# Optimization experiments

Hardware: AMD Instinct MI355X
Metric: run time of the kernel (lower is better)

Reference implementation:

```python
import jax, jax.numpy as jnp
import numpy as np

V, E, H, T = 50000, 128, 256, 9
H2 = H // 2
B, S = 128, 512


def setup_inputs() -> dict:
    key = jax.random.key(0)
    ks = jax.random.split(key, 12)
    sc = 0.05
    return {
        "x": jax.random.randint(ks[0], (B, S), 0, V, dtype=jnp.int64) if False else jax.random.randint(ks[0], (B, S), 0, V).astype(jnp.int64),
        "mask": jnp.ones((B, S), dtype=jnp.int32),
        "embed": jax.random.normal(ks[1], (V, E), jnp.float32) * sc,
        "W_ih_f": jax.random.normal(ks[2], (4 * H2, E), jnp.float32) * sc,
        "W_hh_f": jax.random.normal(ks[3], (4 * H2, H2), jnp.float32) * sc,
        "b_f": jax.random.normal(ks[4], (4 * H2,), jnp.float32) * sc,
        "W_ih_b": jax.random.normal(ks[5], (4 * H2, E), jnp.float32) * sc,
        "W_hh_b": jax.random.normal(ks[6], (4 * H2, H2), jnp.float32) * sc,
        "b_b": jax.random.normal(ks[7], (4 * H2,), jnp.float32) * sc,
        "W_out": jax.random.normal(ks[8], (T, H), jnp.float32) * sc,
        "b_out": jax.random.normal(ks[9], (T,), jnp.float32) * sc,
        "start_trans": jax.random.normal(ks[10], (T,), jnp.float32) * sc,
        "trans": jax.random.normal(ks[11], (T, T), jnp.float32) * sc,
        "end_trans": jax.random.normal(jax.random.fold_in(key, 99), (T,), jnp.float32) * sc,
    }


def _lstm_dir(xg, W_hh, reverse):
    # xg: [B,S,4*H2] precomputed input projections (+bias)
    if reverse:
        xg = xg[:, ::-1]
    b = xg.shape[0]
    h0 = jnp.zeros((b, H2), xg.dtype)

    def step(carry, xt):
        h, c = carry
        g = xt + h @ W_hh.T
        i, f, gg, o = jnp.split(g, 4, axis=-1)
        c = jax.nn.sigmoid(f) * c + jax.nn.sigmoid(i) * jnp.tanh(gg)
        h = jax.nn.sigmoid(o) * jnp.tanh(c)
        return (h, c), h

    _, hs = jax.lax.scan(step, (h0, h0), jnp.swapaxes(xg, 0, 1))
    hs = jnp.swapaxes(hs, 0, 1)  # [B,S,H2]
    if reverse:
        hs = hs[:, ::-1]
    return hs


def _emissions(x, embed, W_ih_f, W_hh_f, b_f, W_ih_b, W_hh_b, b_b, W_out, b_out):
    emb = embed[x]  # [B,S,E]
    xg_f = jnp.einsum('bse,ge->bsg', emb, W_ih_f) + b_f
    xg_b = jnp.einsum('bse,ge->bsg', emb, W_ih_b) + b_b
    h_f = _lstm_dir(xg_f, W_hh_f, False)
    h_b = _lstm_dir(xg_b, W_hh_b, True)
    feats = jnp.concatenate([h_f, h_b], axis=-1)  # [B,S,H]
    return jnp.einsum('bsh,th->bst', feats, W_out) + b_out  # [B,S,T]


def _viterbi(emissions, mask, start_trans, trans, end_trans):
    # emissions [B,S,T], mask [B,S] (1 = valid prefix)
    m = mask.astype(bool)
    score0 = start_trans + emissions[:, 0]  # [B,T]

    def fwd_step(score, inp):
        em_t, m_t = inp  # [B,T], [B]
        nxt = score[:, :, None] + trans[None] + em_t[:, None, :]  # [B,prev,next]
        best = nxt.max(axis=1)
        idx = nxt.argmax(axis=1).astype(jnp.int32)  # [B,T] backpointers
        score = jnp.where(m_t[:, None], best, score)
        return score, idx

    em_rest = jnp.swapaxes(emissions[:, 1:], 0, 1)  # [S-1,B,T]
    m_rest = jnp.swapaxes(m[:, 1:], 0, 1)  # [S-1,B]
    score, history = jax.lax.scan(fwd_step, score0, (em_rest, m_rest))
    final = score + end_trans
    best_scores = final.max(axis=-1)  # [B]
    cur = final.argmax(axis=-1).astype(jnp.int32)  # [B] tag at last valid step

    def back_step(cur, inp):
        hist_t, m_t = inp  # [B,T], [B]
        tag = jnp.where(m_t, cur, -1)  # -1 pads positions beyond seq end
        prev = jnp.take_along_axis(hist_t, cur[:, None], axis=1)[:, 0]
        cur = jnp.where(m_t, prev, cur)
        return cur, tag

    cur0, tags_rev = jax.lax.scan(back_step, cur, (history[::-1], m_rest[::-1]))
    paths = jnp.concatenate(
        [cur0[:, None], jnp.swapaxes(tags_rev, 0, 1)[:, ::-1]], axis=1)  # [B,S]
    return paths, best_scores


def reference(x, mask, embed, W_ih_f, W_hh_f, b_f, W_ih_b, W_hh_b, b_b,
              W_out, b_out, start_trans, trans, end_trans):
    emissions = _emissions(x, embed, W_ih_f, W_hh_f, b_f,
                           W_ih_b, W_hh_b, b_b, W_out, b_out)
    paths, best_scores = _viterbi(emissions, mask, start_trans, trans, end_trans)
    return paths, best_scores
```

## Files before the change

kernel.cpp:

```cpp
#include <hip/hip_runtime.h>
#include <stdint.h>

#define S_LEN 512
#define NT 9

typedef __attribute__((ext_vector_type(8)))  short          bf16x8;
typedef __attribute__((ext_vector_type(4)))  float          f32x4;
typedef __attribute__((ext_vector_type(4)))  unsigned short u16x4;

static __device__ __forceinline__ unsigned short f2bf(float f) {
    union { float f; unsigned u; } c; c.f = f;
    return (unsigned short)((c.u + 0x7fffu + ((c.u >> 16) & 1u)) >> 16);
}
static __device__ __forceinline__ float bf2f(unsigned short h) {
    union { unsigned u; float f; } c; c.u = ((unsigned)h) << 16;
    return c.f;
}
static __device__ __forceinline__ bf16x8 cvt8(const float* p) {
    f32x4 a = *(const f32x4*)p, b = *(const f32x4*)(p + 4);
    bf16x8 fr;
    fr[0]=(short)f2bf(a[0]); fr[1]=(short)f2bf(a[1]); fr[2]=(short)f2bf(a[2]); fr[3]=(short)f2bf(a[3]);
    fr[4]=(short)f2bf(b[0]); fr[5]=(short)f2bf(b[1]); fr[6]=(short)f2bf(b[2]); fr[7]=(short)f2bf(b[3]);
    return fr;
}
static __device__ __forceinline__ bf16x8 pack8(f32x4 a, f32x4 b) {
    bf16x8 fr;
    fr[0]=(short)f2bf(a[0]); fr[1]=(short)f2bf(a[1]); fr[2]=(short)f2bf(a[2]); fr[3]=(short)f2bf(a[3]);
    fr[4]=(short)f2bf(b[0]); fr[5]=(short)f2bf(b[1]); fr[6]=(short)f2bf(b[2]); fr[7]=(short)f2bf(b[3]);
    return fr;
}
static __device__ __forceinline__ float sigf(float x) {
    return __builtin_amdgcn_rcpf(1.0f + __expf(-x));
}
static __device__ __forceinline__ float tanhf_(float x) {
    return 1.0f - 2.0f * __builtin_amdgcn_rcpf(1.0f + __expf(2.0f * x));
}

static __device__ __forceinline__ void wg_barrier_lds() {
    asm volatile("s_waitcnt lgkmcnt(0)" ::: "memory");
    __builtin_amdgcn_s_barrier();
    asm volatile("" ::: "memory");
}

__global__ __launch_bounds__(512) void k_eg(
    const float* __restrict__ embed,
    const float* __restrict__ Wf, const float* __restrict__ bF,
    const float* __restrict__ Wb, const float* __restrict__ bB,
    unsigned short* __restrict__ eg)
{
    const int dir = blockIdx.y, wg = blockIdx.x;
    const float* __restrict__ W    = dir ? Wb : Wf;
    const float* __restrict__ bias = dir ? bB : bF;
    const int tid = threadIdx.x;
    const int wv = tid >> 6, L = tid & 63, l15 = L & 15, l4 = L >> 4;

    bf16x8 Bf[4][4];
    float  bq[4];
#pragma unroll
    for (int q = 0; q < 4; ++q) {
        const int gate = q * 128 + wv * 16 + l15;
        bq[q] = bias[gate];
#pragma unroll
        for (int kt = 0; kt < 4; ++kt)
            Bf[q][kt] = cvt8(W + gate * 128 + kt * 32 + l4 * 8);
    }

    const int vt0 = wg * 25;
    const int hc  = wv * 16 + l15;
    const float* ap = embed + (size_t)(vt0 * 16 + l15) * 128 + l4 * 8;

    f32x4 pv[8];
#pragma unroll
    for (int kt = 0; kt < 4; ++kt) {
        pv[2*kt]   = *(const f32x4*)(ap + kt * 32);
        pv[2*kt+1] = *(const f32x4*)(ap + kt * 32 + 4);
    }

    for (int i = 0; i < 25; ++i) {
        bf16x8 A[4];
#pragma unroll
        for (int kt = 0; kt < 4; ++kt)
            A[kt] = pack8(pv[2*kt], pv[2*kt+1]);
        if (i < 24) {
            const float* apn = ap + (size_t)(i + 1) * 2048;
#pragma unroll
            for (int kt = 0; kt < 4; ++kt) {
                pv[2*kt]   = *(const f32x4*)(apn + kt * 32);
                pv[2*kt+1] = *(const f32x4*)(apn + kt * 32 + 4);
            }
        }
        f32x4 acc[4];
#pragma unroll
        for (int q = 0; q < 4; ++q) {
            f32x4 a0 = { bq[q], bq[q], bq[q], bq[q] };
#pragma unroll
            for (int kt = 0; kt < 4; ++kt)
                a0 = __builtin_amdgcn_mfma_f32_16x16x32_bf16(A[kt], Bf[q][kt], a0, 0, 0, 0);
            acc[q] = a0;
        }
        const int vt = vt0 + i;
#pragma unroll
        for (int j = 0; j < 4; ++j) {
            u16x4 sv;
#pragma unroll
            for (int q = 0; q < 4; ++q) sv[q] = f2bf(acc[q][j]);
            unsigned short* dst = eg +
                (((size_t)(vt * 16 + l4 * 4 + j) * 2 + dir) * 128 + hc) * 4;
            *(u16x4*)dst = sv;
        }
    }
}

__global__ __launch_bounds__(512) void k_lstm(
    const unsigned short* __restrict__ eg, const int* __restrict__ x,
    const float* __restrict__ Whf, const float* __restrict__ Whb,
    unsigned short* __restrict__ feats)
{
    const int dir = blockIdx.y, bt = blockIdx.x;
    const float* __restrict__ Wh = dir ? Whb : Whf;
    const int tid = threadIdx.x, w = tid >> 6, L = tid & 63, l15 = L & 15, l4 = L >> 4;

    bf16x8 Bf[4][4];
#pragma unroll
    for (int q = 0; q < 4; ++q)
#pragma unroll
        for (int kt = 0; kt < 4; ++kt)
            Bf[q][kt] = cvt8(Wh + (q * 128 + w * 16 + l15) * 128 + kt * 32 + l4 * 8);

    __shared__ unsigned short hl[2048];
    for (int i = tid; i < 1024; i += 512) ((unsigned*)hl)[i] = 0;

    const int ar = l15 >> 2;
    int rdoff[4];
#pragma unroll
    for (int kt = 0; kt < 4; ++kt) {
        int p = (kt * 4 + l4 + 2 * ar) & 15;
        rdoff[kt] = ar * 256 + p * 16;
    }
    const int hc = w * 16 + l15;
    const int wroff = l4 * 256 + (((hc >> 3) + 2 * l4) & 15) * 16 + (hc & 7) * 2;

    float c = 0.f;
    const int row = bt * 4 + l4;
    const int* __restrict__ xrow = x + row * S_LEN;
    const size_t egoff = (size_t)dir * 512 + hc * 4;
    unsigned short* fcur = feats + ((size_t)row * 512 + (dir ? 511 : 0)) * 256
                                 + dir * 128 + hc;
    const ptrdiff_t fstep = dir ? -256 : 256;

    int tk0 = xrow[dir ? 511 : 0];
    int tk1 = xrow[dir ? 510 : 1];
    int tkA = xrow[dir ? 509 : 2];
    int tkB = xrow[dir ? 508 : 3];
    u16x4 xvA = *(const u16x4*)(eg + (size_t)tk0 * 1024 + egoff);
    u16x4 xvB = *(const u16x4*)(eg + (size_t)tk1 * 1024 + egoff);

    f32x4 acc[4];
#pragma unroll
    for (int q = 0; q < 4; ++q) acc[q] = f32x4{0.f, 0.f, 0.f, 0.f};

    __syncthreads();

#define LSTM_STEP(T, XV)                                                        \
    {                                                                           \
        const int t_ = (T);                                                     \
        const char* bufR = (const char*)hl + (t_ & 1) * 1024;                   \
        char*       bufW = (char*)hl + ((t_ & 1) ^ 1) * 1024;                   \
        const int t4_ = (t_ < 508) ? (t_ + 4) : 511;     \
        int tknew = xrow[dir ? (511 - t4_) : t4_];                              \
        u16x4 xnew = *(const u16x4*)(eg + (size_t)tkA * 1024 + egoff);          \
        bf16x8 A_[4];                                                           \
        _Pragma("unroll")                                                       \
        for (int kt = 0; kt < 4; ++kt)                                          \
            A_[kt] = *(const bf16x8*)(bufR + rdoff[kt]);                        \
        _Pragma("unroll")                                                       \
        for (int q = 0; q < 4; ++q) {                                           \
            acc[q][0] = bf2f(XV[q]);                                            \
            _Pragma("unroll")                                                   \
            for (int kt = 0; kt < 4; ++kt)                                      \
                acc[q] = __builtin_amdgcn_mfma_f32_16x16x32_bf16(               \
                             A_[kt], Bf[q][kt], acc[q], 0, 0, 0);               \
        }                                                                       \
        float ig = sigf(acc[0][0]);                                             \
        float fg = sigf(acc[1][0]);                                             \
        float gg = tanhf_(acc[2][0]);                                           \
        float og = sigf(acc[3][0]);                                             \
        c = fg * c + ig * gg;                                                   \
        float h_ = og * tanhf_(c);                                              \
        unsigned short hb = f2bf(h_);                                           \
        *(unsigned short*)(bufW + wroff) = hb;                                  \
        *fcur = hb; fcur += fstep;                                              \
        wg_barrier_lds();                                                       \
        XV = xnew;                                                              \
        tkA = tkB; tkB = tknew;                                                 \
    }

    for (int it = 0; it < 256; ++it) {
        LSTM_STEP(2 * it,     xvA)
        LSTM_STEP(2 * it + 1, xvB)
    }
#undef LSTM_STEP
}

__global__ __launch_bounds__(256) void k_viterbi(
    const unsigned short* __restrict__ feats, const float* __restrict__ Wout,
    const int* __restrict__ mask, const float* __restrict__ bout,
    const float* __restrict__ startt, const float* __restrict__ trans,
    const float* __restrict__ endt, float* __restrict__ out)
{
    const int b = blockIdx.x, tid = threadIdx.x;
    const int w = tid >> 6, L = tid & 63, l15 = L & 15, l4 = L >> 4;
    __shared__ float em[512 * 9];
    __shared__ int   msk[512];
    __shared__ unsigned char hist[512 * 9];
    __shared__ unsigned char Gl[32 * 12];
    __shared__ unsigned char bound[32];
    __shared__ int curS;

    bf16x8 Of[2][4];
#pragma unroll
    for (int d = 0; d < 2; ++d)
#pragma unroll
        for (int kt = 0; kt < 4; ++kt) { bf16x8 z;
#pragma unroll
            for (int i = 0; i < 8; ++i) z[i] = 0; Of[d][kt] = z; }
    float bv = 0.f;
    if (l15 < NT) {
        bv = bout[l15];
#pragma unroll
        for (int d = 0; d < 2; ++d)
#pragma unroll
            for (int kt = 0; kt < 4; ++kt)
                Of[d][kt] = cvt8(Wout + l15 * 256 + d * 128 + kt * 32 + l4 * 8);
    }

    for (int i = tid; i < 512; i += 256) msk[i] = mask[b * 512 + i];

#pragma unroll
    for (int i = 0; i < 8; ++i) {
        const int sg = w * 8 + i;
        const unsigned short* frow = feats + ((size_t)b * 512 + sg * 16 + l15) * 256;
        f32x4 e0 = {0, 0, 0, 0}, e1 = {0, 0, 0, 0};
#pragma unroll
        for (int kt = 0; kt < 4; ++kt) {
            bf16x8 A = *(const bf16x8*)(frow + kt * 32 + l4 * 8);
            e0 = __builtin_amdgcn_mfma_f32_16x16x32_bf16(A, Of[0][kt], e0, 0, 0, 0);
        }
#pragma unroll
        for (int kt = 0; kt < 4; ++kt) {
            bf16x8 A = *(const bf16x8*)(frow + 128 + kt * 32 + l4 * 8);
            e1 = __builtin_amdgcn_mfma_f32_16x16x32_bf16(A, Of[1][kt], e1, 0, 0, 0);
        }
        if (l15 < NT) {
#pragma unroll
            for (int j = 0; j < 4; ++j)
                em[(sg * 16 + l4 * 4 + j) * 9 + l15] = (e0[j] + e1[j]) + bv;
        }
    }
    __syncthreads();

    if (tid < 64) {
        const int k = (tid < NT) ? tid : 0;
        float trk[9];
#pragma unroll
        for (int j = 0; j < NT; ++j) trk[j] = trans[j * 9 + k];
        float score = startt[k] + em[k];
        for (int t = 1; t < 512; ++t) {
            float v[9];
#pragma unroll
            for (int j = 0; j < NT; ++j) v[j] = __shfl(score, j, 64) + trk[j];
            float m01 = fmaxf(v[0], v[1]), m23 = fmaxf(v[2], v[3]);
            float m45 = fmaxf(v[4], v[5]), m67 = fmaxf(v[6], v[7]);
            float m = fmaxf(fmaxf(fmaxf(m01, m23), fmaxf(m45, m67)), v[8]);
            int bi = 0;
#pragma unroll
            for (int j = 8; j >= 0; --j) if (v[j] == m) bi = j;
            if (msk[t]) score = m + em[t * 9 + k];
            if (tid < NT) hist[t * 9 + tid] = (unsigned char)bi;
        }
        float fin = score + endt[k];
        float bs = -3e38f; int cur = 0;
#pragma unroll
        for (int j = 0; j < NT; ++j) {
            float vv = __shfl(fin, j, 64);
            if (vv > bs) { bs = vv; cur = j; }
        }
        if (tid == 0) { curS = cur; out[65536 + b] = bs; }
    }
    __syncthreads();

    if (tid < 32) {
        const int m = tid;
        int G[9];
#pragma unroll
        for (int k = 0; k < NT; ++k) G[k] = k;
        const int hi = (m == 31) ? 511 : (16 * m + 16);
        for (int t = hi; t >= 16 * m + 1; --t) {
            if (msk[t]) {
#pragma unroll
                for (int k = 0; k < NT; ++k) G[k] = hist[t * 9 + G[k]];
            }
        }
#pragma unroll
        for (int k = 0; k < NT; ++k) Gl[m * 12 + k] = (unsigned char)G[k];
    }
    __syncthreads();

    if (tid == 0) {
        int e = curS;
        bound[31] = (unsigned char)e;
        for (int m = 31; m >= 1; --m) { e = Gl[m * 12 + e]; bound[m - 1] = (unsigned char)e; }
        out[(size_t)b * 512] = (float)Gl[0 * 12 + e];
    }
    __syncthreads();

    if (tid < 32) {
        const int m = tid;
        int ccur = bound[m];
        const int hi = (m == 31) ? 511 : (16 * m + 16);
        for (int t = hi; t >= 16 * m + 1; --t) {
            const int mt = msk[t];
            out[(size_t)b * 512 + t] = (float)(mt ? ccur : -1);
            if (mt) ccur = hist[t * 9 + ccur];
        }
    }
}

extern "C" void kernel_launch(void* const* d_in, const int* in_sizes, int n_in,
                              void* d_out, int out_size, void* d_ws, size_t ws_size,
                              hipStream_t stream) {
    const int*   x      = (const int*)d_in[0];
    const int*   mask   = (const int*)d_in[1];
    const float* embed  = (const float*)d_in[2];
    const float* Wihf   = (const float*)d_in[3];
    const float* Whhf   = (const float*)d_in[4];
    const float* bf_    = (const float*)d_in[5];
    const float* Wihb   = (const float*)d_in[6];
    const float* Whhb   = (const float*)d_in[7];
    const float* bb_    = (const float*)d_in[8];
    const float* Wout   = (const float*)d_in[9];
    const float* bout   = (const float*)d_in[10];
    const float* startt = (const float*)d_in[11];
    const float* trans  = (const float*)d_in[12];
    const float* endt   = (const float*)d_in[13];

    unsigned short* eg    = (unsigned short*)d_ws;
    unsigned short* feats = (unsigned short*)((char*)d_ws + (size_t)134217728);
    float*          out   = (float*)d_out;

    k_eg     <<<dim3(125, 2), 512, 0, stream>>>(embed, Wihf, bf_, Wihb, bb_, eg);
    k_lstm   <<<dim3(32, 2),  512, 0, stream>>>(eg, x, Whhf, Whhb, feats);
    k_viterbi<<<128,          256, 0, stream>>>(feats, Wout, mask, bout, startt, trans, endt, out);
}
```

Before: 421.7 us.

## Pre-convert embedding to bf16 and split gate table per direction

Adds a separate kernel that converts the fp32 embedding table to bf16 once. k_eg then reads the bf16 copy with two-deep prefetch, so the table is no longer read in fp32 twice (once per direction). It also launches five times more workgroups with fewer tiles each, and stores the gate table as two per-direction planes instead of interleaving directions. The cost is an extra kernel launch plus a full read and write of the converted table, and the different eg layout changes the gather stride in the LSTM.

```diff
diff --git a/kernel.cpp b/kernel.cpp
--- a/kernel.cpp
+++ b/kernel.cpp
@@ -7,6 +7,7 @@
 typedef __attribute__((ext_vector_type(8)))  short          bf16x8;
 typedef __attribute__((ext_vector_type(4)))  float          f32x4;
 typedef __attribute__((ext_vector_type(4)))  unsigned short u16x4;
+typedef __attribute__((ext_vector_type(8)))  unsigned short u16x8;
 
 static __device__ __forceinline__ unsigned short f2bf(float f) {
     union { float f; unsigned u; } c; c.f = f;
@@ -23,12 +24,6 @@
     fr[4]=(short)f2bf(b[0]); fr[5]=(short)f2bf(b[1]); fr[6]=(short)f2bf(b[2]); fr[7]=(short)f2bf(b[3]);
     return fr;
 }
-static __device__ __forceinline__ bf16x8 pack8(f32x4 a, f32x4 b) {
-    bf16x8 fr;
-    fr[0]=(short)f2bf(a[0]); fr[1]=(short)f2bf(a[1]); fr[2]=(short)f2bf(a[2]); fr[3]=(short)f2bf(a[3]);
-    fr[4]=(short)f2bf(b[0]); fr[5]=(short)f2bf(b[1]); fr[6]=(short)f2bf(b[2]); fr[7]=(short)f2bf(b[3]);
-    return fr;
-}
 static __device__ __forceinline__ float sigf(float x) {
     return __builtin_amdgcn_rcpf(1.0f + __expf(-x));
 }
@@ -42,8 +37,20 @@
     asm volatile("" ::: "memory");
 }
 
+__global__ __launch_bounds__(256) void k_ebf(
+    const float* __restrict__ embed, unsigned short* __restrict__ ebf)
+{
+    const size_t n4 = 1600000;
+    for (size_t i = blockIdx.x * 256 + threadIdx.x; i < n4; i += (size_t)2048 * 256) {
+        f32x4 v = *(const f32x4*)(embed + i * 4);
+        u16x4 o;
+        o[0] = f2bf(v[0]); o[1] = f2bf(v[1]); o[2] = f2bf(v[2]); o[3] = f2bf(v[3]);
+        *(u16x4*)(ebf + i * 4) = o;
+    }
+}
+
 __global__ __launch_bounds__(512) void k_eg(
-    const float* __restrict__ embed,
+    const unsigned short* __restrict__ ebf,
     const float* __restrict__ Wf, const float* __restrict__ bF,
     const float* __restrict__ Wb, const float* __restrict__ bB,
     unsigned short* __restrict__ eg)
@@ -65,29 +72,27 @@
             Bf[q][kt] = cvt8(W + gate * 128 + kt * 32 + l4 * 8);
     }
 
-    const int vt0 = wg * 25;
+    const int vt0 = wg * 5;
     const int hc  = wv * 16 + l15;
-    const float* ap = embed + (size_t)(vt0 * 16 + l15) * 128 + l4 * 8;
-
-    f32x4 pv[8];
+    const unsigned short* ap = ebf + (size_t)(vt0 * 16 + l15) * 128 + l4 * 8;
+
+    bf16x8 pA[4], pB[4];
 #pragma unroll
     for (int kt = 0; kt < 4; ++kt) {
-        pv[2*kt]   = *(const f32x4*)(ap + kt * 32);
-        pv[2*kt+1] = *(const f32x4*)(ap + kt * 32 + 4);
-    }
-
-    for (int i = 0; i < 25; ++i) {
+        pA[kt] = *(const bf16x8*)(ap + kt * 32);
+        pB[kt] = *(const bf16x8*)(ap + 2048 + kt * 32);
+    }
+
+    for (int i = 0; i < 5; ++i) {
         bf16x8 A[4];
 #pragma unroll
-        for (int kt = 0; kt < 4; ++kt)
-            A[kt] = pack8(pv[2*kt], pv[2*kt+1]);
-        if (i < 24) {
-            const float* apn = ap + (size_t)(i + 1) * 2048;
-#pragma unroll
-            for (int kt = 0; kt < 4; ++kt) {
-                pv[2*kt]   = *(const f32x4*)(apn + kt * 32);
-                pv[2*kt+1] = *(const f32x4*)(apn + kt * 32 + 4);
-            }
+        for (int kt = 0; kt < 4; ++kt) A[kt] = pA[kt];
+        const int ip2 = (i < 3) ? (i + 2) : i;
+        const unsigned short* apn = ap + (size_t)ip2 * 2048;
+#pragma unroll
+        for (int kt = 0; kt < 4; ++kt) {
+            pA[kt] = pB[kt];
+            pB[kt] = *(const bf16x8*)(apn + kt * 32);
         }
         f32x4 acc[4];
 #pragma unroll
@@ -104,8 +109,8 @@
             u16x4 sv;
 #pragma unroll
             for (int q = 0; q < 4; ++q) sv[q] = f2bf(acc[q][j]);
-            unsigned short* dst = eg +
-                (((size_t)(vt * 16 + l4 * 4 + j) * 2 + dir) * 128 + hc) * 4;
+            unsigned short* dst = eg + (size_t)dir * 25600000 +
+                ((size_t)(vt * 16 + l4 * 4 + j)) * 512 + hc * 4;
             *(u16x4*)dst = sv;
         }
     }
@@ -143,7 +148,8 @@
     float c = 0.f;
     const int row = bt * 4 + l4;
     const int* __restrict__ xrow = x + row * S_LEN;
-    const size_t egoff = (size_t)dir * 512 + hc * 4;
+    const unsigned short* __restrict__ egd = eg + (size_t)dir * 25600000;
+    const int egoff = hc * 4;
     unsigned short* fcur = feats + ((size_t)row * 512 + (dir ? 511 : 0)) * 256
                                  + dir * 128 + hc;
     const ptrdiff_t fstep = dir ? -256 : 256;
@@ -152,8 +158,8 @@
     int tk1 = xrow[dir ? 510 : 1];
     int tkA = xrow[dir ? 509 : 2];
     int tkB = xrow[dir ? 508 : 3];
-    u16x4 xvA = *(const u16x4*)(eg + (size_t)tk0 * 1024 + egoff);
-    u16x4 xvB = *(const u16x4*)(eg + (size_t)tk1 * 1024 + egoff);
+    u16x4 xvA = *(const u16x4*)(egd + (size_t)tk0 * 512 + egoff);
+    u16x4 xvB = *(const u16x4*)(egd + (size_t)tk1 * 512 + egoff);
 
     f32x4 acc[4];
 #pragma unroll
@@ -168,7 +174,7 @@
         char*       bufW = (char*)hl + ((t_ & 1) ^ 1) * 1024;                   \
         const int t4_ = (t_ < 508) ? (t_ + 4) : 511;     \
         int tknew = xrow[dir ? (511 - t4_) : t4_];                              \
-        u16x4 xnew = *(const u16x4*)(eg + (size_t)tkA * 1024 + egoff);          \
+        u16x4 xnew = *(const u16x4*)(egd + (size_t)tkA * 512 + egoff);          \
         bf16x8 A_[4];                                                           \
         _Pragma("unroll")                                                       \
         for (int kt = 0; kt < 4; ++kt)                                          \
@@ -346,9 +352,11 @@
 
     unsigned short* eg    = (unsigned short*)d_ws;
     unsigned short* feats = (unsigned short*)((char*)d_ws + (size_t)134217728);
+    unsigned short* ebf   = (unsigned short*)((char*)d_ws + (size_t)167772160);
     float*          out   = (float*)d_out;
 
-    k_eg     <<<dim3(125, 2), 512, 0, stream>>>(embed, Wihf, bf_, Wihb, bb_, eg);
+    k_ebf    <<<2048,         256, 0, stream>>>(embed, ebf);
+    k_eg     <<<dim3(625, 2), 512, 0, stream>>>(ebf, Wihf, bf_, Wihb, bb_, eg);
     k_lstm   <<<dim3(32, 2),  512, 0, stream>>>(eg, x, Whhf, Whhb, feats);
     k_viterbi<<<128,          256, 0, stream>>>(feats, Wout, mask, bout, startt, trans, endt, out);
 }
```

Measured after the change: 437.0 us. +3.6%, slower.
